# Optimization experiments

Hardware: AMD Instinct MI355X
Metric: run time of the kernel (lower is better)

## Reference

```python
import jax, jax.numpy as jnp
import numpy as np

D, J, K, H = 4, 256, 512, 512  # d, num_output, num_input, num_hidden
B = 1024


def setup_inputs() -> dict:
    key = jax.random.key(0)
    ks = jax.random.split(key, 8)
    x = jax.random.normal(ks[0], (B, K), dtype=jnp.float32)
    # self.w = ((1-0.1)*U + 0.1) / num_input, shape [d, num_output, num_input]
    w = ((0.9 * jax.random.uniform(ks[1], (D, J, K), dtype=jnp.float32) + 0.1) / K)
    # Stacked per-output-MLP params (nn.Linear default init scale 1/sqrt(fan_in))
    s0 = 1.0 / np.sqrt(K)
    s1 = 1.0 / np.sqrt(H)
    W0 = jax.random.uniform(ks[2], (J, H, K), dtype=jnp.float32, minval=-s0, maxval=s0)
    b0 = jax.random.uniform(ks[3], (J, H), dtype=jnp.float32, minval=-s0, maxval=s0)
    W1 = jax.random.uniform(ks[4], (J, H), dtype=jnp.float32, minval=-s1, maxval=s1)  # [J,1,H] squeezed
    b1 = jax.random.uniform(ks[5], (J,), dtype=jnp.float32, minval=-s1, maxval=s1)
    logvar = jnp.ones((D,), dtype=jnp.float32) * -4.0
    return {"x": x, "i": 0, "w": w, "W0": W0, "b0": b0, "W1": W1, "b1": b1, "logvar": logvar}


def reference(x, i, w, W0, b0, W1, b1, logvar):
    # For each output j: mu[:, j] = lin1_j(LeakyReLU(lin0_j(w[i, j] * x)))
    # Fused as a single grouped GEMM over j: fold the mask w[i] into the contraction.
    wi = w[i]                                   # [J, K]
    h = jnp.einsum('jhk,jk,bk->bjh', W0, wi, x) + b0[None, :, :]   # [B, J, H]
    h = jax.nn.leaky_relu(h, negative_slope=0.01)
    mu = jnp.einsum('bjh,jh->bj', h, W1) + b1[None, :]             # [B, J]
    return (mu, logvar)
```

## Files before the change

kernel.cpp:

```cpp
#include <hip/hip_runtime.h>

#define J_ 256
#define K_ 512
#define H_ 512
#define B_ 1024

typedef float f32x4 __attribute__((ext_vector_type(4)));
typedef unsigned int u32x4 __attribute__((ext_vector_type(4)));
typedef unsigned short u16x4 __attribute__((ext_vector_type(4)));
typedef unsigned short u16x8 __attribute__((ext_vector_type(8)));
typedef __bf16 bf16x8 __attribute__((ext_vector_type(8)));

__device__ __forceinline__ unsigned short f2bf(float f) {
    unsigned int u = __float_as_uint(f);
    u += 0x7fffu + ((u >> 16) & 1u);
    return (unsigned short)(u >> 16);
}

__device__ __forceinline__ void gload_lds16(const void* g, void* l) {
    __builtin_amdgcn_global_load_lds(
        (const __attribute__((address_space(1))) unsigned int*)g,
        (__attribute__((address_space(3))) unsigned int*)l, 16, 0, 0);
}

__global__ __launch_bounds__(256) void prep_kernel(
    const float* __restrict__ x, const float* __restrict__ b1,
    const float* __restrict__ logvar, unsigned short* __restrict__ xbf,
    float* __restrict__ out) {
    int t = blockIdx.x * 256 + threadIdx.x;
    {
        f32x4 v = *(const f32x4*)(x + (size_t)t * 4);
        u16x4 o;
        o[0] = f2bf(v[0]); o[1] = f2bf(v[1]); o[2] = f2bf(v[2]); o[3] = f2bf(v[3]);
        *(u16x4*)(xbf + (size_t)t * 4) = o;
    }
    if (t < (B_ * J_) / 4) {
        int b = t >> 6;
        int j4 = (t & 63) << 2;
        f32x4 bb = *(const f32x4*)(b1 + j4);
        *(f32x4*)(out + ((size_t)b << 8) + j4) = bb;
    }
    if (t < 4) out[B_ * J_ + t] = logvar[t];
}

__global__ __launch_bounds__(256) void wprep_kernel(
    const float* __restrict__ W0, const float* __restrict__ wmask,
    const int* __restrict__ ip, unsigned short* __restrict__ w0p) {
    size_t t = (size_t)blockIdx.x * 256 + threadIdx.x;
    size_t e = t * 8;
    int j = (int)(e >> 18);
    int k = (int)(e & (K_ - 1));
    const float* wi = wmask + ((size_t)ip[0] * J_ + j) * K_ + k;
    f32x4 s0 = *(const f32x4*)wi;
    f32x4 s1 = *(const f32x4*)(wi + 4);
    f32x4 a0 = *(const f32x4*)(W0 + e);
    f32x4 a1 = *(const f32x4*)(W0 + e + 4);
    a0 *= s0; a1 *= s1;
    u16x8 o;
    #pragma unroll
    for (int q = 0; q < 4; ++q) { o[q] = f2bf(a0[q]); o[q + 4] = f2bf(a1[q]); }
    *(u16x8*)(w0p + e) = o;
}

__global__ __launch_bounds__(512, 2) void enc_kernel(
    const unsigned short* __restrict__ xbf,
    const unsigned short* __restrict__ w0p,
    const float* __restrict__ b0,
    const float* __restrict__ W1,
    float* __restrict__ out) {
    __shared__ unsigned char ldsA[4 * 16384];
    __shared__ unsigned char ldsB[4 * 16384];

    int p = blockIdx.x;
    int xcd = p & 7;
    int t = p >> 3;
    int j = (xcd << 5) + (t >> 3);
    int inner = t & 7;
    int m0 = (inner >> 1) << 8;
    int h0 = (inner & 1) << 8;

    int tid = threadIdx.x;
    int lane = tid & 63;
    int wv = tid >> 6;
    int wmv = wv >> 2;
    int wnv = wv & 3;
    int lr = lane & 15, lg = lane >> 4;

    int sRow = lane >> 2;
    int sChk = lane & 3;
    int srcChunk = sChk ^ ((lane >> 3) & 3);

    const unsigned short* aSrc = xbf + (size_t)(m0 + wv * 16 + sRow) * K_ + srcChunk * 8;
    const unsigned short* bSrc = w0p + ((size_t)j * H_ + h0 + wv * 16 + sRow) * K_ + srcChunk * 8;
    unsigned char* ldsAw = ldsA + wv * 1024;
    unsigned char* ldsBw = ldsB + wv * 1024;

    int fx = (lg ^ ((lr >> 1) & 3)) << 4;
    const unsigned char* aF = ldsA + (wmv * 128 + lr) * 64 + fx;
    const unsigned char* bF = ldsB + (wnv * 64 + lr) * 64 + fx;

    f32x4 acc[8][4] = {};

#define VMW(n) do { asm volatile("s_waitcnt vmcnt(" #n ")" ::: "memory"); \
                    __builtin_amdgcn_sched_barrier(0); } while (0)
#define LGKM0() do { asm volatile("s_waitcnt lgkmcnt(0)" ::: "memory"); \
                     __builtin_amdgcn_sched_barrier(0); } while (0)
#define BAR() do { __builtin_amdgcn_s_barrier(); \
                   __builtin_amdgcn_sched_barrier(0); } while (0)
#define STG_A(tt) do { int c_ = (tt) & 3; \
    gload_lds16(aSrc + (tt) * 32,                      ldsAw + c_ * 16384); \
    gload_lds16(aSrc + (tt) * 32 + (size_t)128 * K_,   ldsAw + c_ * 16384 + 8192); } while (0)
#define STG_B(tt) do { int c_ = (tt) & 3; \
    gload_lds16(bSrc + (tt) * 32,                      ldsBw + c_ * 16384); \
    gload_lds16(bSrc + (tt) * 32 + (size_t)128 * K_,   ldsBw + c_ * 16384 + 8192); } while (0)
#define LD_A(dst, tt, mf) (dst) = *(const bf16x8*)(aF + ((tt) & 3) * 16384 + (mf) * 1024)
#define LD_B(dst, tt, nf) (dst) = *(const bf16x8*)(bF + ((tt) & 3) * 16384 + (nf) * 1024)
#define MFMAQ(mq, ar) do { __builtin_amdgcn_s_setprio(1); \
    _Pragma("unroll") for (int nf_ = 0; nf_ < 4; ++nf_) { \
      _Pragma("unroll") for (int mf_ = 0; mf_ < 4; ++mf_) \
        acc[(mq) * 4 + mf_][nf_] = __builtin_amdgcn_mfma_f32_16x16x32_bf16( \
            ar[mf_], bC[nf_], acc[(mq) * 4 + mf_][nf_], 0, 0, 0); } \
    __builtin_amdgcn_s_setprio(0); } while (0)

    STG_A(0); STG_B(0); STG_A(1); STG_B(1); STG_A(2); STG_B(2);
    VMW(8);
    BAR();

    bf16x8 aLo[4], bC[4];
    LD_A(aLo[0], 0, 0); LD_A(aLo[1], 0, 1); LD_A(aLo[2], 0, 2); LD_A(aLo[3], 0, 3);
    LD_B(bC[0], 0, 0);  LD_B(bC[1], 0, 1);  LD_B(bC[2], 0, 2);  LD_B(bC[3], 0, 3);

    #pragma unroll
    for (int kt = 0; kt < 16; ++kt) {
        if (kt <= 12) STG_A(kt + 3);
        bf16x8 aHi[4];
        LD_A(aHi[0], kt, 4); LD_A(aHi[1], kt, 5);
        LD_A(aHi[2], kt, 6); LD_A(aHi[3], kt, 7);
        MFMAQ(0, aLo);
        LGKM0();
        if (kt <= 12)      { VMW(6); }
        else if (kt == 13) { VMW(4); }
        else if (kt == 14) { VMW(0); }
        BAR();
        if (kt <= 12) STG_B(kt + 3);
        bf16x8 aN[4], bN[4];
        if (kt < 15) {
            LD_A(aN[0], kt + 1, 0); LD_A(aN[1], kt + 1, 1);
            LD_A(aN[2], kt + 1, 2); LD_A(aN[3], kt + 1, 3);
            LD_B(bN[0], kt + 1, 0); LD_B(bN[1], kt + 1, 1);
            LD_B(bN[2], kt + 1, 2); LD_B(bN[3], kt + 1, 3);
        }
        MFMAQ(1, aHi);
        if (kt < 15) {
            LGKM0();
            BAR();
            aLo[0] = aN[0]; aLo[1] = aN[1]; aLo[2] = aN[2]; aLo[3] = aN[3];
            bC[0] = bN[0];  bC[1] = bN[1];  bC[2] = bN[2];  bC[3] = bN[3];
        }
    }

    float b0v[4], w1v[4];
    #pragma unroll
    for (int nf = 0; nf < 4; ++nf) {
        int col = h0 + (wnv << 6) + (nf << 4) + lr;
        b0v[nf] = b0[(size_t)j * H_ + col];
        w1v[nf] = W1[(size_t)j * H_ + col];
    }
    #pragma unroll
    for (int mf = 0; mf < 8; ++mf) {
        #pragma unroll
        for (int rg = 0; rg < 4; ++rg) {
            float ps = 0.f;
            #pragma unroll
            for (int nf = 0; nf < 4; ++nf) {
                float hv = acc[mf][nf][rg] + b0v[nf];
                hv = hv > 0.f ? hv : 0.01f * hv;
                ps += hv * w1v[nf];
            }
            ps += __shfl_xor(ps, 1);
            ps += __shfl_xor(ps, 2);
            ps += __shfl_xor(ps, 4);
            ps += __shfl_xor(ps, 8);
            if (lr == 0) {
                int row = m0 + (wmv << 7) + (mf << 4) + (lg << 2) + rg;
                atomicAdd(out + (size_t)row * J_ + j, ps);
            }
        }
    }
#undef VMW
#undef LGKM0
#undef BAR
#undef STG_A
#undef STG_B
#undef LD_A
#undef LD_B
#undef MFMAQ
}

__global__ __launch_bounds__(256, 2) void enc_kernel_fb(
    const unsigned short* __restrict__ xbf,
    const float* __restrict__ W0,
    const float* __restrict__ wmask,
    const int* __restrict__ ip,
    const float* __restrict__ b0,
    const float* __restrict__ W1,
    float* __restrict__ out) {
    __shared__ unsigned char ldsA[128 * 128];
    __shared__ unsigned char ldsB[128 * 128];

    int p = blockIdx.x;
    int xcd = p & 7;
    int q = p >> 3;
    int j = (xcd << 5) + (q >> 5);
    int inner = q & 31;
    int m0 = (inner >> 2) << 7;
    int h0 = (inner & 3) << 7;

    int i = ip[0];
    const float* w0j = W0 + (size_t)j * (H_ * K_);
    const float* wij = wmask + ((size_t)i * J_ + j) * K_;

    int tid = threadIdx.x;
    int lane = tid & 63;
    int wv = tid >> 6;
    int wm = wv >> 1, wn = wv & 1;
    int lr = lane & 15, lg = lane >> 4;
    int srow0 = tid >> 3;
    int c = tid & 7;

    f32x4 acc[4][4] = {};

    for (int ks = 0; ks < K_ / 64; ++ks) {
        int k0 = ks * 64;
        #pragma unroll
        for (int it = 0; it < 4; ++it) {
            int r = srow0 + it * 32;
            u32x4 v = *(const u32x4*)(xbf + (size_t)(m0 + r) * K_ + k0 + c * 8);
            *(u32x4*)(ldsA + r * 128 + ((c * 16) ^ ((r & 7) << 4))) = v;
        }
        f32x4 s0 = *(const f32x4*)(wij + k0 + c * 8);
        f32x4 s1 = *(const f32x4*)(wij + k0 + c * 8 + 4);
        #pragma unroll
        for (int it = 0; it < 4; ++it) {
            int hr = srow0 + it * 32;
            const float* src = w0j + (size_t)(h0 + hr) * K_ + k0 + c * 8;
            f32x4 a0 = *(const f32x4*)(src);
            f32x4 a1 = *(const f32x4*)(src + 4);
            a0 *= s0; a1 *= s1;
            u16x8 bvv;
            #pragma unroll
            for (int e = 0; e < 4; ++e) { bvv[e] = f2bf(a0[e]); bvv[e + 4] = f2bf(a1[e]); }
            *(u16x8*)(ldsB + hr * 128 + ((c * 16) ^ ((hr & 7) << 4))) = bvv;
        }
        __syncthreads();
        #pragma unroll
        for (int kf = 0; kf < 2; ++kf) {
            bf16x8 af[4], bfr[4];
            #pragma unroll
            for (int mf = 0; mf < 4; ++mf) {
                int r = (wm << 6) + (mf << 4) + lr;
                af[mf] = *(const bf16x8*)(ldsA + r * 128 +
                          (((kf << 6) + (lg << 4)) ^ ((r & 7) << 4)));
            }
            #pragma unroll
            for (int nf = 0; nf < 4; ++nf) {
                int hrw = (wn << 6) + (nf << 4) + lr;
                bfr[nf] = *(const bf16x8*)(ldsB + hrw * 128 +
                          (((kf << 6) + (lg << 4)) ^ ((hrw & 7) << 4)));
            }
            #pragma unroll
            for (int mf = 0; mf < 4; ++mf)
                #pragma unroll
                for (int nf = 0; nf < 4; ++nf)
                    acc[mf][nf] = __builtin_amdgcn_mfma_f32_16x16x32_bf16(
                        af[mf], bfr[nf], acc[mf][nf], 0, 0, 0);
        }
        __syncthreads();
    }

    float b0v[4], w1v[4];
    #pragma unroll
    for (int nf = 0; nf < 4; ++nf) {
        int h = h0 + (wn << 6) + (nf << 4) + lr;
        b0v[nf] = b0[(size_t)j * H_ + h];
        w1v[nf] = W1[(size_t)j * H_ + h];
    }
    #pragma unroll
    for (int mf = 0; mf < 4; ++mf) {
        #pragma unroll
        for (int rg = 0; rg < 4; ++rg) {
            float ps = 0.f;
            #pragma unroll
            for (int nf = 0; nf < 4; ++nf) {
                float hv = acc[mf][nf][rg] + b0v[nf];
                hv = hv > 0.f ? hv : 0.01f * hv;
                ps += hv * w1v[nf];
            }
            ps += __shfl_xor(ps, 1);
            ps += __shfl_xor(ps, 2);
            ps += __shfl_xor(ps, 4);
            ps += __shfl_xor(ps, 8);
            if (lr == 0) {
                int row = m0 + (wm << 6) + (mf << 4) + (lg << 2) + rg;
                atomicAdd(out + (size_t)row * J_ + j, ps);
            }
        }
    }
}

extern "C" void kernel_launch(void* const* d_in, const int* in_sizes, int n_in,
                              void* d_out, int out_size, void* d_ws, size_t ws_size,
                              hipStream_t stream) {
    const float* x      = (const float*)d_in[0];
    const int*   ip     = (const int*)d_in[1];
    const float* wmask  = (const float*)d_in[2];
    const float* W0     = (const float*)d_in[3];
    const float* b0     = (const float*)d_in[4];
    const float* W1     = (const float*)d_in[5];
    const float* b1     = (const float*)d_in[6];
    const float* logvar = (const float*)d_in[7];
    float* out = (float*)d_out;
    unsigned short* xbf = (unsigned short*)d_ws;
    const size_t xbf_elems = (size_t)B_ * K_;
    const size_t w0p_bytes = (size_t)J_ * H_ * K_ * 2;
    const size_t need = xbf_elems * 2 + w0p_bytes;

    prep_kernel<<<512, 256, 0, stream>>>(x, b1, logvar, xbf, out);
    if (ws_size >= need) {
        unsigned short* w0p = xbf + xbf_elems;
        wprep_kernel<<<32768, 256, 0, stream>>>(W0, wmask, ip, w0p);
        enc_kernel<<<2048, 512, 0, stream>>>(xbf, w0p, b0, W1, out);
    } else {
        enc_kernel_fb<<<8192, 256, 0, stream>>>(xbf, W0, wmask, ip, b0, W1, out);
    }
}
```

Before: 596.3 us.

## Restructure main GEMM loop to K=64 double-buffered tiles with quadrant-interleaved MFMA

The main grouped-GEMM kernel moves from four 32-wide K stages to two 64-wide K buffers in a single 128 KB LDS array, with a new XOR swizzle over 128-byte rows. Each iteration is split into four MFMA quadrants, and the loads for the next tile are interleaved between them under finer barrier and lgkmcnt waits. The aim is fewer outer iterations and better overlap of global-to-LDS copies with MFMA work. The cost is more barriers per iteration and 128 KB of LDS per block, which likely cuts occupancy to one 512-thread block per CU despite launch_bounds(512,2).

```diff
diff --git a/kernel.cpp b/kernel.cpp
--- a/kernel.cpp
+++ b/kernel.cpp
@@ -68,8 +68,7 @@
     const float* __restrict__ b0,
     const float* __restrict__ W1,
     float* __restrict__ out) {
-    __shared__ unsigned char ldsA[4 * 16384];
-    __shared__ unsigned char ldsB[4 * 16384];
+    __shared__ unsigned char lds[131072];
 
     int p = blockIdx.x;
     int xcd = p & 7;
@@ -82,81 +81,91 @@
     int tid = threadIdx.x;
     int lane = tid & 63;
     int wv = tid >> 6;
-    int wmv = wv >> 2;
+    int wm = wv >> 2;
     int wnv = wv & 3;
     int lr = lane & 15, lg = lane >> 4;
-
-    int sRow = lane >> 2;
-    int sChk = lane & 3;
-    int srcChunk = sChk ^ ((lane >> 3) & 3);
-
-    const unsigned short* aSrc = xbf + (size_t)(m0 + wv * 16 + sRow) * K_ + srcChunk * 8;
-    const unsigned short* bSrc = w0p + ((size_t)j * H_ + h0 + wv * 16 + sRow) * K_ + srcChunk * 8;
-    unsigned char* ldsAw = ldsA + wv * 1024;
-    unsigned char* ldsBw = ldsB + wv * 1024;
-
-    int fx = (lg ^ ((lr >> 1) & 3)) << 4;
-    const unsigned char* aF = ldsA + (wmv * 128 + lr) * 64 + fx;
-    const unsigned char* bF = ldsB + (wnv * 64 + lr) * 64 + fx;
-
-    f32x4 acc[8][4] = {};
+    int cBase = lg ^ (lr & 7);
+    int sRow = lane >> 3;
+    int sCh = (lane & 7) ^ sRow;
+
+    const unsigned short* aLane = xbf + (size_t)(m0 + sRow) * K_ + sCh * 8;
+    const unsigned short* bLane = w0p + ((size_t)j * H_ + h0 + sRow) * K_ + sCh * 8;
+
+    const unsigned char* aRd = lds + wm * 16384 + lr * 128;
+    const unsigned char* bRd = lds + 65536 + (wnv >> 1) * 16384 +
+                               ((wnv & 1) * 64 + lr) * 128;
 
 #define VMW(n) do { asm volatile("s_waitcnt vmcnt(" #n ")" ::: "memory"); \
                     __builtin_amdgcn_sched_barrier(0); } while (0)
-#define LGKM0() do { asm volatile("s_waitcnt lgkmcnt(0)" ::: "memory"); \
+#define LGKM(n) do { asm volatile("s_waitcnt lgkmcnt(" #n ")" ::: "memory"); \
                      __builtin_amdgcn_sched_barrier(0); } while (0)
 #define BAR() do { __builtin_amdgcn_s_barrier(); \
                    __builtin_amdgcn_sched_barrier(0); } while (0)
-#define STG_A(tt) do { int c_ = (tt) & 3; \
-    gload_lds16(aSrc + (tt) * 32,                      ldsAw + c_ * 16384); \
-    gload_lds16(aSrc + (tt) * 32 + (size_t)128 * K_,   ldsAw + c_ * 16384 + 8192); } while (0)
-#define STG_B(tt) do { int c_ = (tt) & 3; \
-    gload_lds16(bSrc + (tt) * 32,                      ldsBw + c_ * 16384); \
-    gload_lds16(bSrc + (tt) * 32 + (size_t)128 * K_,   ldsBw + c_ * 16384 + 8192); } while (0)
-#define LD_A(dst, tt, mf) (dst) = *(const bf16x8*)(aF + ((tt) & 3) * 16384 + (mf) * 1024)
-#define LD_B(dst, tt, nf) (dst) = *(const bf16x8*)(bF + ((tt) & 3) * 16384 + (nf) * 1024)
-#define MFMAQ(mq, ar) do { __builtin_amdgcn_s_setprio(1); \
-    _Pragma("unroll") for (int nf_ = 0; nf_ < 4; ++nf_) { \
+#define STG_A(bf, hf, kk) do { \
+    gload_lds16(aLane + (size_t)((hf) * 128 + wv * 8) * K_ + (kk) * 64, \
+                lds + (bf) * 32768 + (hf) * 16384 + wv * 1024); \
+    gload_lds16(aLane + (size_t)((hf) * 128 + 64 + wv * 8) * K_ + (kk) * 64, \
+                lds + (bf) * 32768 + (hf) * 16384 + 8192 + wv * 1024); } while (0)
+#define STG_B(bf, hf, kk) do { \
+    gload_lds16(bLane + (size_t)((hf) * 128 + wv * 8) * K_ + (kk) * 64, \
+                lds + 65536 + (bf) * 32768 + (hf) * 16384 + wv * 1024); \
+    gload_lds16(bLane + (size_t)((hf) * 128 + 64 + wv * 8) * K_ + (kk) * 64, \
+                lds + 65536 + (bf) * 32768 + (hf) * 16384 + 8192 + wv * 1024); } while (0)
+#define LDA(dst, bf, qm, mf, kf) (dst) = *(const bf16x8*)(aRd + (bf) * 32768 + \
+    ((qm) * 64 + (mf) * 16) * 128 + ((cBase ^ ((kf) << 2)) << 4))
+#define LDB(dst, bf, pp, nf, kf) (dst) = *(const bf16x8*)(bRd + (bf) * 32768 + \
+    ((pp) * 32 + (nf) * 16) * 128 + ((cBase ^ ((kf) << 2)) << 4))
+#define MFMA_Q(qm, qn, aR, bR) do { \
+    __builtin_amdgcn_s_setprio(1); \
+    _Pragma("unroll") for (int kf_ = 0; kf_ < 2; ++kf_) \
       _Pragma("unroll") for (int mf_ = 0; mf_ < 4; ++mf_) \
-        acc[(mq) * 4 + mf_][nf_] = __builtin_amdgcn_mfma_f32_16x16x32_bf16( \
-            ar[mf_], bC[nf_], acc[(mq) * 4 + mf_][nf_], 0, 0, 0); } \
+        _Pragma("unroll") for (int nf_ = 0; nf_ < 2; ++nf_) \
+          acc[(qm) * 4 + mf_][(qn) * 2 + nf_] = \
+              __builtin_amdgcn_mfma_f32_16x16x32_bf16( \
+                  aR[kf_][mf_], bR[kf_][nf_], acc[(qm) * 4 + mf_][(qn) * 2 + nf_], 0, 0, 0); \
     __builtin_amdgcn_s_setprio(0); } while (0)
 
-    STG_A(0); STG_B(0); STG_A(1); STG_B(1); STG_A(2); STG_B(2);
-    VMW(8);
-    BAR();
-
-    bf16x8 aLo[4], bC[4];
-    LD_A(aLo[0], 0, 0); LD_A(aLo[1], 0, 1); LD_A(aLo[2], 0, 2); LD_A(aLo[3], 0, 3);
-    LD_B(bC[0], 0, 0);  LD_B(bC[1], 0, 1);  LD_B(bC[2], 0, 2);  LD_B(bC[3], 0, 3);
-
-    #pragma unroll
-    for (int kt = 0; kt < 16; ++kt) {
-        if (kt <= 12) STG_A(kt + 3);
-        bf16x8 aHi[4];
-        LD_A(aHi[0], kt, 4); LD_A(aHi[1], kt, 5);
-        LD_A(aHi[2], kt, 6); LD_A(aHi[3], kt, 7);
-        MFMAQ(0, aLo);
-        LGKM0();
-        if (kt <= 12)      { VMW(6); }
-        else if (kt == 13) { VMW(4); }
-        else if (kt == 14) { VMW(0); }
-        BAR();
-        if (kt <= 12) STG_B(kt + 3);
-        bf16x8 aN[4], bN[4];
-        if (kt < 15) {
-            LD_A(aN[0], kt + 1, 0); LD_A(aN[1], kt + 1, 1);
-            LD_A(aN[2], kt + 1, 2); LD_A(aN[3], kt + 1, 3);
-            LD_B(bN[0], kt + 1, 0); LD_B(bN[1], kt + 1, 1);
-            LD_B(bN[2], kt + 1, 2); LD_B(bN[3], kt + 1, 3);
-        }
-        MFMAQ(1, aHi);
-        if (kt < 15) {
-            LGKM0();
-            BAR();
-            aLo[0] = aN[0]; aLo[1] = aN[1]; aLo[2] = aN[2]; aLo[3] = aN[3];
-            bC[0] = bN[0];  bC[1] = bN[1];  bC[2] = bN[2];  bC[3] = bN[3];
-        }
+    f32x4 acc[8][4] = {};
+    bf16x8 aC[2][4], bL[2][2], bH[2][2];
+
+    STG_A(0, 0, 0); STG_A(0, 1, 0); STG_B(0, 0, 0); STG_B(0, 1, 0);
+    STG_B(1, 0, 1); STG_A(1, 0, 1);
+    VMW(4); BAR();
+
+    #pragma unroll
+    for (int kt = 0; kt < 8; ++kt) {
+        const int bf = kt & 1, bn = bf ^ 1;
+        LDA(aC[0][0], bf, 0, 0, 0); LDA(aC[0][1], bf, 0, 1, 0);
+        LDA(aC[0][2], bf, 0, 2, 0); LDA(aC[0][3], bf, 0, 3, 0);
+        LDA(aC[1][0], bf, 0, 0, 1); LDA(aC[1][1], bf, 0, 1, 1);
+        LDA(aC[1][2], bf, 0, 2, 1); LDA(aC[1][3], bf, 0, 3, 1);
+        LDB(bL[0][0], bf, 0, 0, 0); LDB(bL[0][1], bf, 0, 1, 0);
+        LDB(bL[1][0], bf, 0, 0, 1); LDB(bL[1][1], bf, 0, 1, 1);
+        if (kt < 7) STG_A(bn, 1, kt + 1);
+        LGKM(8);
+        BAR(); LGKM(0);
+        MFMA_Q(0, 0, aC, bL);
+        BAR();
+        LDB(bH[0][0], bf, 1, 0, 0); LDB(bH[0][1], bf, 1, 1, 0);
+        LDB(bH[1][0], bf, 1, 0, 1); LDB(bH[1][1], bf, 1, 1, 1);
+        if (kt < 7) STG_B(bn, 1, kt + 1);
+        BAR(); LGKM(0);
+        MFMA_Q(0, 1, aC, bH);
+        BAR();
+        LDA(aC[0][0], bf, 1, 0, 0); LDA(aC[0][1], bf, 1, 1, 0);
+        LDA(aC[0][2], bf, 1, 2, 0); LDA(aC[0][3], bf, 1, 3, 0);
+        LDA(aC[1][0], bf, 1, 0, 1); LDA(aC[1][1], bf, 1, 1, 1);
+        LDA(aC[1][2], bf, 1, 2, 1); LDA(aC[1][3], bf, 1, 3, 1);
+        if (kt < 6) STG_B(bf, 0, kt + 2);
+        BAR(); LGKM(0);
+        MFMA_Q(1, 0, aC, bL);
+        BAR();
+        if (kt < 6) STG_A(bf, 0, kt + 2);
+        if (kt < 6)      { VMW(4); }
+        else if (kt == 6) { VMW(0); }
+        BAR();
+        MFMA_Q(1, 1, aC, bH);
+        BAR();
     }
 
     float b0v[4], w1v[4];
@@ -182,19 +191,19 @@
             ps += __shfl_xor(ps, 4);
             ps += __shfl_xor(ps, 8);
             if (lr == 0) {
-                int row = m0 + (wmv << 7) + (mf << 4) + (lg << 2) + rg;
+                int row = m0 + (wm << 7) + (mf << 4) + (lg << 2) + rg;
                 atomicAdd(out + (size_t)row * J_ + j, ps);
             }
         }
     }
 #undef VMW
-#undef LGKM0
+#undef LGKM
 #undef BAR
 #undef STG_A
 #undef STG_B
-#undef LD_A
-#undef LD_B
-#undef MFMAQ
+#undef LDA
+#undef LDB
+#undef MFMA_Q
 }
 
 __global__ __launch_bounds__(256, 2) void enc_kernel_fb(
```

Measured after the change: 580.8 us. -2.6%, faster.
